# Kernel optimization log

Hardware: AMD Instinct MI355X
Metric: run time of the kernel (lower is better)

Reference implementation:

```python
import jax, jax.numpy as jnp
import numpy as np
import math

B, T, C, N = 2, 2048, 1024, 16  # batch, seq, h_dim, n_heads
D = C // N

def setup_inputs() -> dict:
    key = jax.random.key(0)
    k1, k2, k3 = jax.random.split(key, 3)
    x = jax.random.normal(k1, (B, T, C), dtype=jnp.float32)
    Wqkv = jax.random.normal(k2, (C, 3 * C), dtype=jnp.float32) * (1.0 / math.sqrt(C))
    bqkv = jnp.zeros((3 * C,), dtype=jnp.float32)
    Wproj = jax.random.normal(k3, (C, C), dtype=jnp.float32) * (1.0 / math.sqrt(C))
    bproj = jnp.zeros((C,), dtype=jnp.float32)
    return {"x": x, "Wqkv": Wqkv, "bqkv": bqkv, "Wproj": Wproj, "bproj": bproj}

def reference(x, Wqkv, bqkv, Wproj, bproj):
    B_, T_, C_ = x.shape
    N_, D_ = N, C_ // N
    qkv = x @ Wqkv + bqkv                                  # (B,T,3C)
    q, k, v = jnp.split(qkv, 3, axis=-1)
    q = q.reshape(B_, T_, N_, D_).transpose(0, 2, 1, 3)    # (B,N,T,D)
    k = k.reshape(B_, T_, N_, D_).transpose(0, 2, 1, 3)
    v = v.reshape(B_, T_, N_, D_).transpose(0, 2, 1, 3)
    # causal mask: lower-triangular ones, broadcast over (B, 1, T, T)
    mask = jnp.tril(jnp.ones((T_, T_), dtype=jnp.float32))[None, None]
    weights = jnp.einsum('bntd,bnsd->bnts', q, k) / math.sqrt(D_)
    # faithful to original: adds tiny 1e-9 to masked entries (NOT -inf)
    weights = weights + (1.0 - mask) * 1e-9
    normalized = jax.nn.softmax(weights, axis=-1)
    attn = jnp.einsum('bnts,bnsd->bntd', normalized, v)    # (B,N,T,D)
    attn = attn.transpose(0, 2, 1, 3).reshape(B_, T_, N_ * D_)
    out = attn @ Wproj + bproj                              # (B,T,C)
    return out
```

## Files before the change

### kernel.cpp

```cpp
#include <hip/hip_runtime.h>
#include <hip/hip_bf16.h>

#define BB 2
#define TT 2048
#define CC 1024
#define NHEAD 16
#define DHEAD 64
#define MM (BB*TT)
#define KVB 128

using bf16 = __hip_bfloat16;
typedef __bf16 bf16x8 __attribute__((ext_vector_type(8)));
typedef __bf16 bf16x4 __attribute__((ext_vector_type(4)));
typedef float f32x4 __attribute__((ext_vector_type(4)));

static __device__ __forceinline__ bf16 f2b(float f) { return __float2bfloat16(f); }
static __device__ __forceinline__ float fast_exp2(float f) { return __builtin_amdgcn_exp2f(f); }

static __device__ __forceinline__ void gload16(const bf16* g, bf16* l) {
  __builtin_amdgcn_global_load_lds((__attribute__((address_space(1))) const void*)g,
                                   (__attribute__((address_space(3))) void*)l, 16, 0, 0);
}

__global__ __launch_bounds__(256)
void k_prep(const float* __restrict__ x, bf16* __restrict__ Xb,
            const float* __restrict__ Wqkv, bf16* __restrict__ WqkvT,
            const float* __restrict__ Wproj, bf16* __restrict__ WprojT)
{
  const int bid = blockIdx.x, tid = threadIdx.x;
  if (bid < 4096) {
    int i = bid * 256 + tid;
    float4 v = reinterpret_cast<const float4*>(x)[i];
    bf16 o[4] = { f2b(v.x), f2b(v.y), f2b(v.z), f2b(v.w) };
    reinterpret_cast<uint2*>(Xb)[i] = *reinterpret_cast<uint2*>(o);
    return;
  }
  __shared__ float tile[32][33];
  const float* W; bf16* WT; int R, Cc, bx, by;
  if (bid < 4096 + 3072) {
    int b2 = bid - 4096;  W = Wqkv;  WT = WqkvT;  R = CC; Cc = 3*CC;
    bx = b2 % 96; by = b2 / 96;
  } else {
    int b3 = bid - 7168;  W = Wproj; WT = WprojT; R = CC; Cc = CC;
    bx = b3 % 32; by = b3 / 32;
  }
  int c0 = bx * 32, r0 = by * 32;
  int tx = tid & 31, ty = tid >> 5;
#pragma unroll
  for (int i = 0; i < 4; ++i)
    tile[ty + 8*i][tx] = W[(size_t)(r0 + ty + 8*i) * Cc + c0 + tx];
  __syncthreads();
#pragma unroll
  for (int i = 0; i < 4; ++i)
    WT[(size_t)(c0 + ty + 8*i) * R + r0 + tx] = f2b(tile[tx][ty + 8*i]);
}

__global__ void k_vtrans(const bf16* __restrict__ V, bf16* __restrict__ VT) {
  __shared__ bf16 tile[32][33];
  const int bn = blockIdx.z;
  const int d0 = blockIdx.x * 32, t0 = blockIdx.y * 32;
  const size_t base = (size_t)bn * TT * DHEAD;
  int tx = threadIdx.x, ty = threadIdx.y;
#pragma unroll
  for (int i = 0; i < 4; ++i)
    tile[ty + 8*i][tx] = V[base + (size_t)(t0 + ty + 8*i) * DHEAD + d0 + tx];
  __syncthreads();
#pragma unroll
  for (int i = 0; i < 4; ++i)
    VT[base + (size_t)(d0 + ty + 8*i) * TT + t0 + tx] = tile[tx][ty + 8*i];
}

#define NTK 32
__global__ __launch_bounds__(512, 1)
void k_gemm_qkv(const bf16* __restrict__ Ag, const bf16* __restrict__ Bg,
                const float* __restrict__ bias,
                bf16* __restrict__ Qb, bf16* __restrict__ Kb, bf16* __restrict__ Vb)
{
  const int tid = threadIdx.x;
  const int w = tid >> 6, l = tid & 63;
  const int l16 = l & 15, l4 = l >> 4;
  const int wr = w >> 2, wc = w & 3;

  const int flat = blockIdx.x;
  const int swz = (flat & 7) * 24 + (flat >> 3);
  const int bx = swz / 16, by = swz % 16;
  const int m0 = by * 256, n0 = bx * 256;

  __shared__ __align__(16) bf16 sm[32768];

  f32x4 acc[8][4];
#pragma unroll
  for (int m = 0; m < 8; ++m)
#pragma unroll
    for (int n = 0; n < 4; ++n) acc[m][n] = 0.f;

  const int srow = tid >> 2;
  const int scol = ((tid & 3) ^ ((tid >> 3) & 3)) * 8;

#define STAGE(buf, kt) do {                                                          \
    const int kb = (kt) * 32 + scol;                                                 \
    gload16(&Ag[(size_t)(m0 +       srow) * CC + kb], &sm[(buf)*16384         + w*512]); \
    gload16(&Ag[(size_t)(m0 + 128 + srow) * CC + kb], &sm[(buf)*16384 +  4096 + w*512]); \
    gload16(&Bg[(size_t)(n0 +       srow) * CC + kb], &sm[(buf)*16384 +  8192 + w*512]); \
    gload16(&Bg[(size_t)(n0 + 128 + srow) * CC + kb], &sm[(buf)*16384 + 12288 + w*512]); \
  } while (0)

  STAGE(0, 0);
  STAGE(1, 1);
  asm volatile("s_waitcnt vmcnt(4)" ::: "memory");
  __builtin_amdgcn_s_barrier();

  const int slotA = (l4 ^ ((l16 >> 1) & 3)) * 8;
  const int aoff = wr * 4096 + l16 * 32 + slotA;
  const int boff = 8192 + (wc >> 1) * 4096 + ((wc & 1) * 64 + l16) * 32 + slotA;

  for (int kt = 0; kt < NTK; ++kt) {
    const int buf = kt & 1;
    const int base = buf * 16384;

    bf16x8 bfr[4], af[4];
#pragma unroll
    for (int n = 0; n < 4; ++n)
      bfr[n] = *reinterpret_cast<const bf16x8*>(&sm[base + boff + n*512]);
#pragma unroll
    for (int m = 0; m < 4; ++m)
      af[m] = *reinterpret_cast<const bf16x8*>(&sm[base + aoff + m*512]);
    __builtin_amdgcn_s_setprio(1);
#pragma unroll
    for (int m = 0; m < 4; ++m)
#pragma unroll
      for (int n = 0; n < 4; ++n)
        acc[m][n] = __builtin_amdgcn_mfma_f32_16x16x32_bf16(af[m], bfr[n], acc[m][n], 0, 0, 0);
    __builtin_amdgcn_s_setprio(0);
#pragma unroll
    for (int m = 0; m < 4; ++m)
      af[m] = *reinterpret_cast<const bf16x8*>(&sm[base + aoff + (m+4)*512]);
    __builtin_amdgcn_s_setprio(1);
#pragma unroll
    for (int m = 0; m < 4; ++m)
#pragma unroll
      for (int n = 0; n < 4; ++n)
        acc[m+4][n] = __builtin_amdgcn_mfma_f32_16x16x32_bf16(af[m], bfr[n], acc[m+4][n], 0, 0, 0);
    __builtin_amdgcn_s_setprio(0);

    __builtin_amdgcn_s_barrier();
    if (kt + 2 < NTK) {
      STAGE(buf, kt + 2);
      asm volatile("s_waitcnt vmcnt(4)" ::: "memory");
    } else {
      asm volatile("s_waitcnt vmcnt(0)" ::: "memory");
    }
    __builtin_amdgcn_s_barrier();
  }
#undef STAGE

  const int ccol = n0 + wc * 64;
  const int which = ccol >> 10;
  bf16* __restrict__ dst = (which == 0) ? Qb : (which == 1) ? Kb : Vb;
  const float qsc = (which == 0) ? 0.125f * 1.4426950408889634f : 1.0f;
#pragma unroll
  for (int m = 0; m < 8; ++m)
#pragma unroll
    for (int n = 0; n < 4; ++n) {
      int gc = ccol + n*16 + l16;
      float bv = bias[gc];
      int c = gc & (CC-1), head = c >> 6, d = c & 63;
#pragma unroll
      for (int j = 0; j < 4; ++j) {
        int gr = m0 + wr*128 + m*16 + l4*4 + j;
        int b = gr >> 11, t = gr & (TT-1);
        dst[(((size_t)b*NHEAD + head)*TT + t)*DHEAD + d] = f2b((acc[m][n][j] + bv) * qsc);
      }
    }
}

__global__ __launch_bounds__(256)
void k_gemm_proj(const bf16* __restrict__ A, const bf16* __restrict__ Bt,
                 const float* __restrict__ bias, float* __restrict__ outF, int K)
{
  const int tid  = threadIdx.x;
  const int wave = tid >> 6, lane = tid & 63;
  const int l16 = lane & 15, l4 = lane >> 4;
  const int wr = wave >> 1, wc = wave & 1;

  const int gx = gridDim.x;
  const int flat = blockIdx.y * gx + blockIdx.x;
  const int cpx = (gx * gridDim.y) >> 3;
  const int swz = (flat & 7) * cpx + (flat >> 3);
  const int bx = swz % gx, by = swz / gx;
  const int m0 = by * 128, n0 = bx * 128;

  __shared__ __align__(16) bf16 As[128*32];
  __shared__ __align__(16) bf16 Bs[128*32];

  f32x4 acc[4][4];
#pragma unroll
  for (int m = 0; m < 4; ++m)
#pragma unroll
    for (int n = 0; n < 4; ++n) acc[m][n] = 0.f;

  const int sr = tid >> 2;
  const int sc = (tid & 3) * 8;

  for (int k0 = 0; k0 < K; k0 += 32) {
    __syncthreads();
#pragma unroll
    for (int i = 0; i < 2; ++i) {
      gload16(&A [(size_t)(m0 + i*64 + sr) * K + k0 + sc], &As[i*2048 + tid*8]);
      gload16(&Bt[(size_t)(n0 + i*64 + sr) * K + k0 + sc], &Bs[i*2048 + tid*8]);
    }
    __syncthreads();
    bf16x8 af[4], bfr[4];
#pragma unroll
    for (int m = 0; m < 4; ++m)
      af[m] = *reinterpret_cast<const bf16x8*>(&As[(wr*64 + m*16 + l16)*32 + l4*8]);
#pragma unroll
    for (int n = 0; n < 4; ++n)
      bfr[n] = *reinterpret_cast<const bf16x8*>(&Bs[(wc*64 + n*16 + l16)*32 + l4*8]);
#pragma unroll
    for (int m = 0; m < 4; ++m)
#pragma unroll
      for (int n = 0; n < 4; ++n)
        acc[m][n] = __builtin_amdgcn_mfma_f32_16x16x32_bf16(af[m], bfr[n], acc[m][n], 0, 0, 0);
  }

#pragma unroll
  for (int m = 0; m < 4; ++m)
#pragma unroll
    for (int n = 0; n < 4; ++n)
#pragma unroll
      for (int j = 0; j < 4; ++j) {
        int gr = m0 + wr*64 + m*16 + l4*4 + j;
        int gc = n0 + wc*64 + n*16 + l16;
        outF[(size_t)gr * CC + gc] = acc[m][n][j] + bias[gc];
      }
}

__global__ __launch_bounds__(512, 2)
void k_attn(const bf16* __restrict__ Qg, const bf16* __restrict__ Kg,
            const bf16* __restrict__ VTg, bf16* __restrict__ Aout)
{
  const int tid  = threadIdx.x;
  const int wave = tid >> 6, lane = tid & 63;
  const int l16 = lane & 15, l4 = lane >> 4;

  const int flat = blockIdx.x;
  const int xcd = flat & 7, i6 = flat >> 3;
  const int bn = xcd*4 + (i6 >> 4);
  const int q0 = (i6 & 15) * 128;
  const int b = bn >> 4, h = bn & (NHEAD-1);

  __shared__ __align__(16) bf16 Ks[KVB][72];
  __shared__ __align__(16) bf16 Vt[DHEAD][136];
  __shared__ __align__(16) bf16 Pl[8][16][136];

  const size_t hb = (size_t)bn * TT * DHEAD;
  const bf16* __restrict__ Kbase = Kg + hb;
  const bf16* __restrict__ Vbase = VTg + hb;

  bf16x8 qf[2];
#pragma unroll
  for (int kk = 0; kk < 2; ++kk)
    qf[kk] = *reinterpret_cast<const bf16x8*>(
        &Qg[hb + (size_t)(q0 + wave*16 + l16) * DHEAD + kk*32 + l4*8]);

  f32x4 o[4];
#pragma unroll
  for (int n = 0; n < 4; ++n) o[n] = 0.f;
  float mrun = -1e30f, lrun = 0.f;

  const int krow = tid >> 2, kcol = (tid & 3) * 16;
  const int vrow = tid >> 3, vcol = (tid & 7) * 16;

  bf16x8 kreg[2], vreg[2];
#pragma unroll
  for (int i = 0; i < 2; ++i) {
    kreg[i] = *reinterpret_cast<const bf16x8*>(&Kbase[(size_t)krow * DHEAD + kcol + 8*i]);
    vreg[i] = *reinterpret_cast<const bf16x8*>(&Vbase[(size_t)vrow * TT + vcol + 8*i]);
  }
#pragma unroll
  for (int i = 0; i < 2; ++i) {
    *reinterpret_cast<bf16x8*>(&Ks[krow][kcol + 8*i]) = kreg[i];
    *reinterpret_cast<bf16x8*>(&Vt[vrow][vcol + 8*i]) = vreg[i];
  }

  for (int t0 = 0; t0 < TT; t0 += KVB) {
    __syncthreads();
    const bool more = (t0 + KVB < TT);
    if (more) {
#pragma unroll
      for (int i = 0; i < 2; ++i) {
        kreg[i] = *reinterpret_cast<const bf16x8*>(
            &Kbase[(size_t)(t0 + KVB + krow) * DHEAD + kcol + 8*i]);
        vreg[i] = *reinterpret_cast<const bf16x8*>(
            &Vbase[(size_t)vrow * TT + t0 + KVB + vcol + 8*i]);
      }
    }

    f32x4 s[8];
#pragma unroll
    for (int n = 0; n < 8; ++n) s[n] = 0.f;
    __builtin_amdgcn_s_setprio(1);
#pragma unroll
    for (int n = 0; n < 8; ++n) {
      bf16x8 kf0 = *reinterpret_cast<const bf16x8*>(&Ks[n*16 + l16][l4*8]);
      bf16x8 kf1 = *reinterpret_cast<const bf16x8*>(&Ks[n*16 + l16][32 + l4*8]);
      s[n] = __builtin_amdgcn_mfma_f32_16x16x32_bf16(kf0, qf[0], s[n], 0, 0, 0);
      s[n] = __builtin_amdgcn_mfma_f32_16x16x32_bf16(kf1, qf[1], s[n], 0, 0, 0);
    }
    __builtin_amdgcn_s_setprio(0);

    float pm = s[0][0];
#pragma unroll
    for (int n = 0; n < 8; ++n)
#pragma unroll
      for (int j = 0; j < 4; ++j) pm = fmaxf(pm, s[n][j]);
    pm = fmaxf(pm, __shfl_xor(pm, 16, 64));
    pm = fmaxf(pm, __shfl_xor(pm, 32, 64));

    if (!__all(pm <= mrun + 8.f)) {
      float mn = fmaxf(mrun, pm);
      float corr = fast_exp2(mrun - mn);
      mrun = mn;
      lrun *= corr;
      float cj[4];
#pragma unroll
      for (int j = 0; j < 4; ++j)
        cj[j] = __shfl(corr, ((lane >> 4) << 2) + j, 64);
#pragma unroll
      for (int n = 0; n < 4; ++n)
#pragma unroll
        for (int j = 0; j < 4; ++j) o[n][j] *= cj[j];
    }

    float psum = 0.f;
#pragma unroll
    for (int n = 0; n < 8; ++n) {
      bf16x4 pk;
#pragma unroll
      for (int j = 0; j < 4; ++j) {
        float pv = fast_exp2(s[n][j] - mrun);
        psum += pv;
        pk[j] = (__bf16)pv;
      }
      *reinterpret_cast<bf16x4*>(&Pl[wave][l16][n*16 + l4*4]) = pk;
    }
    psum += __shfl_xor(psum, 16, 64);
    psum += __shfl_xor(psum, 32, 64);
    lrun += psum;

    bf16x8 pf[4];
#pragma unroll
    for (int kk = 0; kk < 4; ++kk)
      pf[kk] = *reinterpret_cast<const bf16x8*>(&Pl[wave][l16][kk*32 + l4*8]);
    __builtin_amdgcn_s_setprio(1);
#pragma unroll
    for (int n = 0; n < 4; ++n)
#pragma unroll
      for (int kk = 0; kk < 4; ++kk) {
        bf16x8 vf = *reinterpret_cast<const bf16x8*>(&Vt[n*16 + l16][kk*32 + l4*8]);
        o[n] = __builtin_amdgcn_mfma_f32_16x16x32_bf16(pf[kk], vf, o[n], 0, 0, 0);
      }
    __builtin_amdgcn_s_setprio(0);

    __syncthreads();
    if (more) {
#pragma unroll
      for (int i = 0; i < 2; ++i) {
        *reinterpret_cast<bf16x8*>(&Ks[krow][kcol + 8*i]) = kreg[i];
        *reinterpret_cast<bf16x8*>(&Vt[vrow][vcol + 8*i]) = vreg[i];
      }
    }
  }

  float linv = 1.0f / lrun;
  float lj[4];
#pragma unroll
  for (int j = 0; j < 4; ++j)
    lj[j] = __shfl(linv, ((lane >> 4) << 2) + j, 64);
#pragma unroll
  for (int j = 0; j < 4; ++j) {
    int gt = q0 + wave*16 + l4*4 + j;
#pragma unroll
    for (int n = 0; n < 4; ++n)
      Aout[((size_t)(b*TT + gt))*CC + h*DHEAD + n*16 + l16] = f2b(o[n][j] * lj[j]);
  }
}

extern "C" void kernel_launch(void* const* d_in, const int* in_sizes, int n_in,
                              void* d_out, int out_size, void* d_ws, size_t ws_size,
                              hipStream_t stream)
{
  const float* x     = (const float*)d_in[0];
  const float* Wqkv  = (const float*)d_in[1];
  const float* bqkv  = (const float*)d_in[2];
  const float* Wproj = (const float*)d_in[3];
  const float* bproj = (const float*)d_in[4];
  float* out = (float*)d_out;

  char* p = (char*)d_ws;
  bf16* Xb     = (bf16*)p;  p += (size_t)MM*CC*2;
  bf16* WqkvT  = (bf16*)p;  p += (size_t)3*CC*CC*2;
  bf16* WprojT = (bf16*)p;  p += (size_t)CC*CC*2;
  bf16* Qb     = (bf16*)p;  p += (size_t)MM*CC*2;
  bf16* Kb     = (bf16*)p;  p += (size_t)MM*CC*2;
  bf16* Vb     = (bf16*)p;  p += (size_t)MM*CC*2;
  bf16* Attn   = (bf16*)p;  p += (size_t)MM*CC*2;
  bf16* VTb    = Xb;

  k_prep<<<8192, 256, 0, stream>>>(x, Xb, Wqkv, WqkvT, Wproj, WprojT);
  k_gemm_qkv<<<192, 512, 0, stream>>>(Xb, WqkvT, bqkv, Qb, Kb, Vb);
  k_vtrans<<<dim3(DHEAD/32, TT/32, BB*NHEAD), dim3(32, 8), 0, stream>>>(Vb, VTb);
  k_attn<<<512, 512, 0, stream>>>(Qb, Kb, VTb, Attn);
  k_gemm_proj<<<dim3(CC/128, MM/128), 256, 0, stream>>>(Attn, WprojT, bproj, out, CC);
}
```

Measured before the change: 136.6 us.

## Shrink QKV GEMM tile to 128x256, triple-buffer loads, coarsen prep conversion

```diff
diff --git a/kernel.cpp b/kernel.cpp
--- a/kernel.cpp
+++ b/kernel.cpp
@@ -27,22 +27,29 @@
             const float* __restrict__ Wqkv, bf16* __restrict__ WqkvT,
             const float* __restrict__ Wproj, bf16* __restrict__ WprojT)
 {
-  const int bid = blockIdx.x, tid = threadIdx.x;
-  if (bid < 4096) {
-    int i = bid * 256 + tid;
-    float4 v = reinterpret_cast<const float4*>(x)[i];
-    bf16 o[4] = { f2b(v.x), f2b(v.y), f2b(v.z), f2b(v.w) };
-    reinterpret_cast<uint2*>(Xb)[i] = *reinterpret_cast<uint2*>(o);
+  int bid = blockIdx.x;
+  const int tid = threadIdx.x;
+  if (bid < 1024) {
+    int base = bid * 1024 + tid;
+#pragma unroll
+    for (int k = 0; k < 4; ++k) {
+      int i = base + k * 256;
+      float4 v = reinterpret_cast<const float4*>(x)[i];
+      bf16 o[4] = { f2b(v.x), f2b(v.y), f2b(v.z), f2b(v.w) };
+      reinterpret_cast<uint2*>(Xb)[i] = *reinterpret_cast<uint2*>(o);
+    }
     return;
   }
+  bid -= 1024;
   __shared__ float tile[32][33];
   const float* W; bf16* WT; int R, Cc, bx, by;
-  if (bid < 4096 + 3072) {
-    int b2 = bid - 4096;  W = Wqkv;  WT = WqkvT;  R = CC; Cc = 3*CC;
-    bx = b2 % 96; by = b2 / 96;
+  if (bid < 3072) {
+    W = Wqkv;  WT = WqkvT;  R = CC; Cc = 3*CC;
+    bx = bid % 96; by = bid / 96;
   } else {
-    int b3 = bid - 7168;  W = Wproj; WT = WprojT; R = CC; Cc = CC;
-    bx = b3 % 32; by = b3 / 32;
+    bid -= 3072;
+    W = Wproj; WT = WprojT; R = CC; Cc = CC;
+    bx = bid % 32; by = bid / 32;
   }
   int c0 = bx * 32, r0 = by * 32;
   int tx = tid & 31, ty = tid >> 5;
@@ -71,7 +78,7 @@
 }
 
 #define NTK 32
-__global__ __launch_bounds__(512, 1)
+__global__ __launch_bounds__(512, 2)
 void k_gemm_qkv(const bf16* __restrict__ Ag, const bf16* __restrict__ Bg,
                 const float* __restrict__ bias,
                 bf16* __restrict__ Qb, bf16* __restrict__ Kb, bf16* __restrict__ Vb)
@@ -82,49 +89,50 @@
   const int wr = w >> 2, wc = w & 3;
 
   const int flat = blockIdx.x;
-  const int swz = (flat & 7) * 24 + (flat >> 3);
-  const int bx = swz / 16, by = swz % 16;
-  const int m0 = by * 256, n0 = bx * 256;
-
-  __shared__ __align__(16) bf16 sm[32768];
-
-  f32x4 acc[8][4];
-#pragma unroll
-  for (int m = 0; m < 8; ++m)
+  const int xcd = flat & 7, local = flat >> 3;
+  const int bx = (xcd & 1) * 6 + local % 6;
+  const int by = (xcd >> 1) * 8 + local / 6;
+  const int m0 = by * 128, n0 = bx * 256;
+
+  __shared__ __align__(16) bf16 sm[36864];
+
+  f32x4 acc[4][4];
+#pragma unroll
+  for (int m = 0; m < 4; ++m)
 #pragma unroll
     for (int n = 0; n < 4; ++n) acc[m][n] = 0.f;
 
   const int srow = tid >> 2;
   const int scol = ((tid & 3) ^ ((tid >> 3) & 3)) * 8;
 
-#define STAGE(buf, kt) do {                                                          \
-    const int kb = (kt) * 32 + scol;                                                 \
-    gload16(&Ag[(size_t)(m0 +       srow) * CC + kb], &sm[(buf)*16384         + w*512]); \
-    gload16(&Ag[(size_t)(m0 + 128 + srow) * CC + kb], &sm[(buf)*16384 +  4096 + w*512]); \
-    gload16(&Bg[(size_t)(n0 +       srow) * CC + kb], &sm[(buf)*16384 +  8192 + w*512]); \
-    gload16(&Bg[(size_t)(n0 + 128 + srow) * CC + kb], &sm[(buf)*16384 + 12288 + w*512]); \
+#define STAGE(buf, kt) do {                                                            \
+    const int kb = (kt) * 32 + scol;                                                   \
+    gload16(&Ag[(size_t)(m0 +       srow) * CC + kb], &sm[(buf)*12288        + w*512]);\
+    gload16(&Bg[(size_t)(n0 +       srow) * CC + kb], &sm[(buf)*12288 + 4096 + w*512]);\
+    gload16(&Bg[(size_t)(n0 + 128 + srow) * CC + kb], &sm[(buf)*12288 + 8192 + w*512]);\
   } while (0)
 
   STAGE(0, 0);
   STAGE(1, 1);
-  asm volatile("s_waitcnt vmcnt(4)" ::: "memory");
+  STAGE(2, 2);
+  asm volatile("s_waitcnt vmcnt(6)" ::: "memory");
   __builtin_amdgcn_s_barrier();
 
   const int slotA = (l4 ^ ((l16 >> 1) & 3)) * 8;
-  const int aoff = wr * 4096 + l16 * 32 + slotA;
-  const int boff = 8192 + (wc >> 1) * 4096 + ((wc & 1) * 64 + l16) * 32 + slotA;
-
+  const int aoff = wr * 2048 + l16 * 32 + slotA;
+  const int boff = 4096 + wc * 2048 + l16 * 32 + slotA;
+
+  int rb = 0;
   for (int kt = 0; kt < NTK; ++kt) {
-    const int buf = kt & 1;
-    const int base = buf * 16384;
-
-    bf16x8 bfr[4], af[4];
+    const int base = rb * 12288;
+
+    bf16x8 af[4], bfr[4];
+#pragma unroll
+    for (int m = 0; m < 4; ++m)
+      af[m] = *reinterpret_cast<const bf16x8*>(&sm[base + aoff + m*512]);
 #pragma unroll
     for (int n = 0; n < 4; ++n)
       bfr[n] = *reinterpret_cast<const bf16x8*>(&sm[base + boff + n*512]);
-#pragma unroll
-    for (int m = 0; m < 4; ++m)
-      af[m] = *reinterpret_cast<const bf16x8*>(&sm[base + aoff + m*512]);
     __builtin_amdgcn_s_setprio(1);
 #pragma unroll
     for (int m = 0; m < 4; ++m)
@@ -132,25 +140,18 @@
       for (int n = 0; n < 4; ++n)
         acc[m][n] = __builtin_amdgcn_mfma_f32_16x16x32_bf16(af[m], bfr[n], acc[m][n], 0, 0, 0);
     __builtin_amdgcn_s_setprio(0);
-#pragma unroll
-    for (int m = 0; m < 4; ++m)
-      af[m] = *reinterpret_cast<const bf16x8*>(&sm[base + aoff + (m+4)*512]);
-    __builtin_amdgcn_s_setprio(1);
-#pragma unroll
-    for (int m = 0; m < 4; ++m)
-#pragma unroll
-      for (int n = 0; n < 4; ++n)
-        acc[m+4][n] = __builtin_amdgcn_mfma_f32_16x16x32_bf16(af[m], bfr[n], acc[m+4][n], 0, 0, 0);
-    __builtin_amdgcn_s_setprio(0);
 
     __builtin_amdgcn_s_barrier();
-    if (kt + 2 < NTK) {
-      STAGE(buf, kt + 2);
-      asm volatile("s_waitcnt vmcnt(4)" ::: "memory");
-    } else {
+    if (kt + 3 < NTK) {
+      STAGE(rb, kt + 3);
+      asm volatile("s_waitcnt vmcnt(6)" ::: "memory");
+    } else if (kt + 2 < NTK) {
+      asm volatile("s_waitcnt vmcnt(3)" ::: "memory");
+    } else if (kt + 1 < NTK) {
       asm volatile("s_waitcnt vmcnt(0)" ::: "memory");
     }
     __builtin_amdgcn_s_barrier();
+    rb = (rb + 1 == 3) ? 0 : rb + 1;
   }
 #undef STAGE
 
@@ -159,7 +160,7 @@
   bf16* __restrict__ dst = (which == 0) ? Qb : (which == 1) ? Kb : Vb;
   const float qsc = (which == 0) ? 0.125f * 1.4426950408889634f : 1.0f;
 #pragma unroll
-  for (int m = 0; m < 8; ++m)
+  for (int m = 0; m < 4; ++m)
 #pragma unroll
     for (int n = 0; n < 4; ++n) {
       int gc = ccol + n*16 + l16;
@@ -167,7 +168,7 @@
       int c = gc & (CC-1), head = c >> 6, d = c & 63;
 #pragma unroll
       for (int j = 0; j < 4; ++j) {
-        int gr = m0 + wr*128 + m*16 + l4*4 + j;
+        int gr = m0 + wr*64 + m*16 + l4*4 + j;
         int b = gr >> 11, t = gr & (TT-1);
         dst[(((size_t)b*NHEAD + head)*TT + t)*DHEAD + d] = f2b((acc[m][n][j] + bv) * qsc);
       }
@@ -408,8 +409,8 @@
   bf16* Attn   = (bf16*)p;  p += (size_t)MM*CC*2;
   bf16* VTb    = Xb;
 
-  k_prep<<<8192, 256, 0, stream>>>(x, Xb, Wqkv, WqkvT, Wproj, WprojT);
-  k_gemm_qkv<<<192, 512, 0, stream>>>(Xb, WqkvT, bqkv, Qb, Kb, Vb);
+  k_prep<<<5120, 256, 0, stream>>>(x, Xb, Wqkv, WqkvT, Wproj, WprojT);
+  k_gemm_qkv<<<384, 512, 0, stream>>>(Xb, WqkvT, bqkv, Qb, Kb, Vb);
   k_vtrans<<<dim3(DHEAD/32, TT/32, BB*NHEAD), dim3(32, 8), 0, stream>>>(Vb, VTb);
   k_attn<<<512, 512, 0, stream>>>(Qb, Kb, VTb, Attn);
   k_gemm_proj<<<dim3(CC/128, MM/128), 256, 0, stream>>>(Attn, WprojT, bproj, out, CC);
```

After: 134.6 us. Within noise of the previous version (-1.4%).
